# Kernel optimization log

Hardware: AMD Instinct MI355X
Metric: run time of the kernel (lower is better)

Reference implementation:

```python
import jax, jax.numpy as jnp
import numpy as np

N_NODES = 100000
N_EDGES = 1600000
D_IN = 128
D_OUT = 128


def setup_inputs() -> dict:
    key = jax.random.key(0)
    ks = jax.random.split(key, 8)
    x = jax.random.normal(ks[0], (N_NODES, D_IN), dtype=jnp.float32)
    edge_index = jax.random.randint(ks[1], (2, N_EDGES), 0, N_NODES, dtype=jnp.int64)
    s1 = 1.0 / np.sqrt(D_IN)
    s2 = 1.0 / np.sqrt(D_OUT)
    # SAGEConv: lin_l acts on aggregated neighbors (has bias), lin_r on self (no bias)
    Wl1 = jax.random.uniform(ks[2], (D_OUT, D_IN), jnp.float32, -s1, s1)
    Wr1 = jax.random.uniform(ks[3], (D_OUT, D_IN), jnp.float32, -s1, s1)
    b1 = jnp.zeros((D_OUT,), jnp.float32)
    Wl2 = jax.random.uniform(ks[4], (D_OUT, D_OUT), jnp.float32, -s2, s2)
    Wr2 = jax.random.uniform(ks[5], (D_OUT, D_OUT), jnp.float32, -s2, s2)
    b2 = jnp.zeros((D_OUT,), jnp.float32)
    return {"x": x, "edge_index": edge_index, "Wl1": Wl1, "Wr1": Wr1, "b1": b1,
            "Wl2": Wl2, "Wr2": Wr2, "b2": b2}


def _sage_conv(x, src, dst, Wl, Wr, b, n_nodes):
    # mean aggregation of source features at destination nodes
    agg = jax.ops.segment_sum(x[src], dst, num_segments=n_nodes)  # [N, d]
    deg = jax.ops.segment_sum(jnp.ones((src.shape[0],), x.dtype), dst, num_segments=n_nodes)
    mean = agg / jnp.maximum(deg, 1.0)[:, None]  # isolated nodes -> 0 (PyG scatter-mean)
    return mean @ Wl.T + b + x @ Wr.T


def reference(x, edge_index, Wl1, Wr1, b1, Wl2, Wr2, b2):
    src, dst = edge_index[0], edge_index[1]
    n = x.shape[0]
    h = _sage_conv(x, src, dst, Wl1, Wr1, b1, n)
    h = _sage_conv(h, src, dst, Wl2, Wr2, b2, n)
    return h
```

## Files before the change

kernel.cpp:

```cpp
#include <hip/hip_runtime.h>
#include <hip/hip_bf16.h>

#define D 128
#define SCAN_CHUNK 1024
#define TE 4096

typedef __attribute__((ext_vector_type(8))) short bf16x8;
typedef __attribute__((ext_vector_type(4))) float f32x4;
typedef __attribute__((ext_vector_type(2))) float f32x2;

__device__ __forceinline__ bool ei_is64(const int* ei32) {
    return (ei32[1] | ei32[3] | ei32[5] | ei32[7]) == 0;
}
__device__ __forceinline__ int get_idx(const void* ei, bool is64, long long pos) {
    return is64 ? (int)((const long long*)ei)[pos] : ((const int*)ei)[pos];
}

__global__ __launch_bounds__(256) void prep_kernel(
    const float* __restrict__ x, __hip_bfloat16* __restrict__ xb,
    unsigned* __restrict__ xq, long long ND, int ncvt,
    const float* __restrict__ Wl1, const float* __restrict__ Wr1,
    const float* __restrict__ Wl2, const float* __restrict__ Wr2,
    ushort* __restrict__ Wf1, ushort* __restrict__ Wf2,
    const void* __restrict__ ei, int E, int NB, int NBLK, int SH,
    int* __restrict__ histT) {
    __shared__ int h[512];
    const int t = threadIdx.x;
    int bid = blockIdx.x;

    if (bid < ncvt) {
        long long i = ((long long)bid * 256 + t) * 4;
        if (i + 3 < ND) {
            float4 v = *reinterpret_cast<const float4*>(x + i);
            __hip_bfloat16 o[4];
            o[0] = __float2bfloat16(v.x); o[1] = __float2bfloat16(v.y);
            o[2] = __float2bfloat16(v.z); o[3] = __float2bfloat16(v.w);
            *reinterpret_cast<ushort4*>(xb + i) = *reinterpret_cast<ushort4*>(o);
            int pk = __builtin_amdgcn_cvt_pk_fp8_f32(v.x, v.y, 0, false);
            pk = __builtin_amdgcn_cvt_pk_fp8_f32(v.z, v.w, pk, true);
            xq[i >> 2] = (unsigned)pk;
        } else {
            for (; i < ND; ++i) {
                float v = x[i];
                xb[i] = __float2bfloat16(v);
                int pk = __builtin_amdgcn_cvt_pk_fp8_f32(v, v, 0, false);
                ((unsigned char*)xq)[i] = (unsigned char)(pk & 0xff);
            }
        }
        return;
    }
    bid -= ncvt;
    if (bid < 32) {
        int gid = bid * 256 + t;
        int id = gid & 4095;
        const float* Wl = Wl1; const float* Wr = Wr1; ushort* Wf = Wf1;
        if (gid >= 4096) { Wl = Wl2; Wr = Wr2; Wf = Wf2; }
        int lane = id & 63, s = (id >> 6) & 7, j = id >> 9;
        int c = j * 16 + (lane & 15);
        int k = s * 32 + ((lane >> 4) << 3);
        const float* src = (k < 128) ? (Wl + c * 128 + k) : (Wr + c * 128 + (k - 128));
        float4 v0 = *reinterpret_cast<const float4*>(src);
        float4 v1 = *reinterpret_cast<const float4*>(src + 4);
        __hip_bfloat16 o[8];
        o[0] = __float2bfloat16(v0.x); o[1] = __float2bfloat16(v0.y);
        o[2] = __float2bfloat16(v0.z); o[3] = __float2bfloat16(v0.w);
        o[4] = __float2bfloat16(v1.x); o[5] = __float2bfloat16(v1.y);
        o[6] = __float2bfloat16(v1.z); o[7] = __float2bfloat16(v1.w);
        *reinterpret_cast<uint4*>(Wf + (size_t)id * 8) = *reinterpret_cast<uint4*>(o);
        return;
    }
    bid -= 32;
    for (int b = t; b < 512; b += 256) h[b] = 0;
    bool is64 = ei_is64((const int*)ei);
    __syncthreads();
    const int base = bid * TE;
    for (int i = t; i < TE; i += 256) {
        int e = base + i;
        if (e < E) {
            int d = get_idx(ei, is64, (long long)E + e);
            atomicAdd(&h[d >> SH], 1);
        }
    }
    __syncthreads();
    for (int b = t; b < NB; b += 256) histT[b * NBLK + bid] = h[b];
}

__global__ __launch_bounds__(256) void scan_partial_kernel(int* __restrict__ arr, int Ntot,
                                                           int* __restrict__ bsum) {
    __shared__ int s[SCAN_CHUNK];
    int base = blockIdx.x * SCAN_CHUNK;
    for (int j = threadIdx.x; j < SCAN_CHUNK; j += 256) {
        int i = base + j;
        s[j] = (i < Ntot) ? arr[i] : 0;
    }
    __syncthreads();
    if (threadIdx.x == 0) {
        int run = 0;
        for (int j = 0; j < SCAN_CHUNK; ++j) { int t = s[j]; s[j] = run; run += t; }
        bsum[blockIdx.x] = run;
    }
    __syncthreads();
    for (int j = threadIdx.x; j < SCAN_CHUNK; j += 256) {
        int i = base + j;
        if (i < Ntot) arr[i] = s[j];
    }
}

__global__ __launch_bounds__(256) void scan_top_kernel(int* __restrict__ bsum, int nb) {
    __shared__ int s[1024];
    const int t = threadIdx.x;
    for (int j = t; j < nb; j += 256) s[j] = bsum[j];
    __syncthreads();
    if (t == 0) {
        int run = 0;
        for (int j = 0; j < nb; ++j) { int v = s[j]; s[j] = run; run += v; }
    }
    __syncthreads();
    for (int j = t; j < nb; j += 256) bsum[j] = s[j];
}

__global__ __launch_bounds__(256) void part_scatter_kernel(const void* __restrict__ ei, int E,
                                                           int NB, int NBLK, int SH,
                                                           const int* __restrict__ histT,
                                                           const int* __restrict__ bsum,
                                                           unsigned* __restrict__ ebuf) {
    __shared__ int cur[512];
    const int t = threadIdx.x;
    bool is64 = ei_is64((const int*)ei);
    for (int b = t; b < NB; b += 256) {
        int idx = b * NBLK + blockIdx.x;
        cur[b] = histT[idx] + bsum[idx >> 10];
    }
    __syncthreads();
    const int base = blockIdx.x * TE;
    for (int i = t; i < TE; i += 256) {
        int e = base + i;
        if (e < E) {
            int s = get_idx(ei, is64, e);
            int d = get_idx(ei, is64, (long long)E + e);
            int pos = atomicAdd(&cur[d >> SH], 1);
            ebuf[pos] = (unsigned)s | ((unsigned)(d & ((1 << SH) - 1)) << 24);
        }
    }
}

__global__ __launch_bounds__(256) void bucket_csr_kernel(const unsigned* __restrict__ ebuf,
                                                         const int* __restrict__ histT,
                                                         const int* __restrict__ bsum,
                                                         int NB, int NBLK, int SH, int E,
                                                         int N, int* __restrict__ rs,
                                                         int* __restrict__ col) {
    const int b = blockIdx.x, t = threadIdx.x;
    const int nodes = 1 << SH;
    __shared__ int h[256];
    __shared__ int cur[256];
    __shared__ int sse[2];
    if (t == 0) {
        int i0 = b * NBLK;
        sse[0] = histT[i0] + bsum[i0 >> 10];
        if (b + 1 < NB) {
            int i1 = (b + 1) * NBLK;
            sse[1] = histT[i1] + bsum[i1 >> 10];
        } else {
            sse[1] = E;
        }
    }
    for (int l = t; l < nodes; l += 256) h[l] = 0;
    __syncthreads();
    const int bstart = sse[0], bend = sse[1];
    for (int i = bstart + t; i < bend; i += 256) {
        atomicAdd(&h[ebuf[i] >> 24], 1);
    }
    __syncthreads();
    for (int off = 1; off < nodes; off <<= 1) {
        int v = 0;
        if (t < nodes && t >= off) v = h[t - off];
        __syncthreads();
        if (t < nodes && t >= off) h[t] += v;
        __syncthreads();
    }
    const int node0 = b << SH;
    if (t < nodes) {
        int node = node0 + t;
        if (node < N) rs[node] = bstart + h[t];
        cur[t] = bstart + (t ? h[t - 1] : 0);
    }
    __syncthreads();
    for (int i = bstart + t; i < bend; i += 256) {
        unsigned ed = ebuf[i];
        int pos = atomicAdd(&cur[ed >> 24], 1);
        col[pos] = (int)(ed & 0xFFFFFFu);
    }
}

__global__ __launch_bounds__(256) void aggregate_mean_fp8_kernel(
    const unsigned char* __restrict__ xq, const int* __restrict__ rs,
    const int* __restrict__ col, ushort* __restrict__ outm, int N) {
    int t = threadIdx.x;
    int v = blockIdx.x * 4 + (t >> 6);
    if (v >= N) return;
    int lane = t & 63, q = lane >> 4, lc = lane & 15;
    int start = v ? rs[v - 1] : 0, end = rs[v];
    f32x2 a0 = {0.f, 0.f}, a1 = {0.f, 0.f}, a2 = {0.f, 0.f}, a3 = {0.f, 0.f};
    int e = start + q;
    for (; e + 4 < end; e += 8) {
        int s0 = col[e], s1 = col[e + 4];
        uint2 d0 = *reinterpret_cast<const uint2*>(xq + (size_t)s0 * D + lc * 8);
        uint2 d1 = *reinterpret_cast<const uint2*>(xq + (size_t)s1 * D + lc * 8);
        a0 += __builtin_amdgcn_cvt_pk_f32_fp8((int)d0.x, false);
        a1 += __builtin_amdgcn_cvt_pk_f32_fp8((int)d0.x, true);
        a2 += __builtin_amdgcn_cvt_pk_f32_fp8((int)d0.y, false);
        a3 += __builtin_amdgcn_cvt_pk_f32_fp8((int)d0.y, true);
        a0 += __builtin_amdgcn_cvt_pk_f32_fp8((int)d1.x, false);
        a1 += __builtin_amdgcn_cvt_pk_f32_fp8((int)d1.x, true);
        a2 += __builtin_amdgcn_cvt_pk_f32_fp8((int)d1.y, false);
        a3 += __builtin_amdgcn_cvt_pk_f32_fp8((int)d1.y, true);
    }
    if (e < end) {
        int s0 = col[e];
        uint2 d0 = *reinterpret_cast<const uint2*>(xq + (size_t)s0 * D + lc * 8);
        a0 += __builtin_amdgcn_cvt_pk_f32_fp8((int)d0.x, false);
        a1 += __builtin_amdgcn_cvt_pk_f32_fp8((int)d0.x, true);
        a2 += __builtin_amdgcn_cvt_pk_f32_fp8((int)d0.y, false);
        a3 += __builtin_amdgcn_cvt_pk_f32_fp8((int)d0.y, true);
    }
    float a[8] = {a0.x, a0.y, a1.x, a1.y, a2.x, a2.y, a3.x, a3.y};
#pragma unroll
    for (int i = 0; i < 8; ++i) {
        a[i] += __shfl_xor(a[i], 16);
        a[i] += __shfl_xor(a[i], 32);
    }
    if (q == 0) {
        float inv = (end > start) ? 1.0f / (float)(end - start) : 0.f;
        __hip_bfloat16 o[8];
#pragma unroll
        for (int i = 0; i < 8; ++i) o[i] = __float2bfloat16(a[i] * inv);
        *reinterpret_cast<uint4*>(outm + (size_t)v * D + lc * 8) =
            *reinterpret_cast<uint4*>(o);
    }
}

template <typename OutT, bool DUAL>
__global__ __launch_bounds__(512) void sage_mfma_kernel(
    const ushort* __restrict__ Ab, const ushort* __restrict__ Sb,
    const ushort* __restrict__ Wf, const float* __restrict__ bias,
    OutT* __restrict__ out, unsigned char* __restrict__ fq, int N) {
    __shared__ uint4 ldsB[4096];
    const int t = threadIdx.x;
    {
        const uint4* g = reinterpret_cast<const uint4*>(Wf);
#pragma unroll
        for (int i = 0; i < 8; ++i) ldsB[t + i * 512] = g[t + i * 512];
    }
    __syncthreads();

    const int lane = t & 63, w = t >> 6;
    const int lm = lane & 15;
    const int ksub = (lane >> 4) * 8;
    const int mbase = blockIdx.x * 128 + w * 16;

    int r0 = mbase + lm;
    if (r0 >= N) r0 = N - 1;

    f32x4 acc[8];
#pragma unroll
    for (int j = 0; j < 8; ++j) {
        float bv = bias[j * 16 + lm];
        acc[j] = {bv, bv, bv, bv};
    }

    const ushort* A0 = Ab + (size_t)r0 * D + ksub;
    const ushort* S0 = Sb + (size_t)r0 * D + ksub;
    const ushort* lB = reinterpret_cast<const ushort*>(ldsB) + lane * 8;

#pragma unroll
    for (int s = 0; s < 8; ++s) {
        bf16x8 a = (s < 4) ? *reinterpret_cast<const bf16x8*>(A0 + s * 32)
                           : *reinterpret_cast<const bf16x8*>(S0 + (s - 4) * 32);
#pragma unroll
        for (int j = 0; j < 8; ++j) {
            bf16x8 b = *reinterpret_cast<const bf16x8*>(lB + (j * 8 + s) * 512);
            acc[j] = __builtin_amdgcn_mfma_f32_16x16x32_bf16(a, b, acc[j], 0, 0, 0);
        }
    }

    const int rr = (lane >> 4) * 4;
#pragma unroll
    for (int r = 0; r < 4; ++r) {
        int row = mbase + rr + r;
        if (row < N) {
#pragma unroll
            for (int j = 0; j < 8; ++j) {
                float val = acc[j][r];
                if constexpr (sizeof(OutT) == 2)
                    out[(size_t)row * D + j * 16 + lm] = __float2bfloat16(val);
                else
                    out[(size_t)row * D + j * 16 + lm] = val;
                if constexpr (DUAL) {
                    int pk = __builtin_amdgcn_cvt_pk_fp8_f32(val, val, 0, false);
                    fq[(size_t)row * D + j * 16 + lm] = (unsigned char)(pk & 0xff);
                }
            }
        }
    }
}

extern "C" void kernel_launch(void* const* d_in, const int* in_sizes, int n_in,
                              void* d_out, int out_size, void* d_ws, size_t ws_size,
                              hipStream_t stream) {
    const float* x   = (const float*)d_in[0];
    const void*  ei  = d_in[1];
    const float* Wl1 = (const float*)d_in[2];
    const float* Wr1 = (const float*)d_in[3];
    const float* b1  = (const float*)d_in[4];
    const float* Wl2 = (const float*)d_in[5];
    const float* Wr2 = (const float*)d_in[6];
    const float* b2  = (const float*)d_in[7];
    float* out = (float*)d_out;

    const int N = in_sizes[0] / D;
    const int E = in_sizes[1] / 2;
    const long long ND = (long long)N * D;

    int SH = 8;
    while (((N + (1 << SH) - 1) >> SH) > 512) ++SH;
    const int NB = (N + (1 << SH) - 1) >> SH;
    const int NBLK = (E + TE - 1) / TE;
    const int Ntot = NB * NBLK;
    const int nb2 = (Ntot + SCAN_CHUNK - 1) / SCAN_CHUNK;

    ushort* meanb = (ushort*)d_ws;
    ushort* h1b   = meanb + ND;
    ushort* Wf1   = h1b + ND;
    ushort* Wf2   = Wf1 + 32768;
    int*    rs    = (int*)(Wf2 + 32768);
    int*    col   = rs + N;
    int*      histT = (int*)meanb;
    int*      bsum  = histT + Ntot;
    unsigned* ebuf  = (unsigned*)h1b;
    ushort*        xb  = (ushort*)d_out;
    unsigned char* xq  = (unsigned char*)d_out + 2 * ND;
    unsigned char* h1q = (unsigned char*)d_out + 3 * ND;

    const int ncvt = (int)((ND / 4 + 255) / 256);

    prep_kernel<<<ncvt + 32 + NBLK, 256, 0, stream>>>(
        x, (__hip_bfloat16*)xb, (unsigned*)xq, ND, ncvt, Wl1, Wr1, Wl2, Wr2,
        Wf1, Wf2, ei, E, NB, NBLK, SH, histT);

    scan_partial_kernel<<<nb2, 256, 0, stream>>>(histT, Ntot, bsum);
    scan_top_kernel<<<1, 256, 0, stream>>>(bsum, nb2);
    part_scatter_kernel<<<NBLK, 256, 0, stream>>>(ei, E, NB, NBLK, SH, histT, bsum, ebuf);
    bucket_csr_kernel<<<NB, 256, 0, stream>>>(ebuf, histT, bsum, NB, NBLK, SH, E, N, rs, col);

    const int agg_grid = (N + 3) / 4;
    const int gemm_grid = (N + 127) / 128;

    aggregate_mean_fp8_kernel<<<agg_grid, 256, 0, stream>>>(xq, rs, col, meanb, N);
    sage_mfma_kernel<__hip_bfloat16, true><<<gemm_grid, 512, 0, stream>>>(
        meanb, xb, Wf1, b1, (__hip_bfloat16*)h1b, h1q, N);

    aggregate_mean_fp8_kernel<<<agg_grid, 256, 0, stream>>>(h1q, rs, col, meanb, N);
    sage_mfma_kernel<float, false><<<gemm_grid, 512, 0, stream>>>(
        meanb, h1b, Wf2, b2, out, nullptr, N);
}
```

Baseline: 200.2 us.

## Drop bf16 copy of x and remap aggregation to one node per 16 lanes

The prep kernel no longer writes a bf16 copy of x. It only produces the fp8 copy, now 8 elements per thread. The first GEMM reads the fp32 x directly and converts it to bf16 in registers, which removes a full write and reread of a bf16 copy of x. The aggregation kernel now gives each node 16 lanes that walk every edge with 4-way unrolled gathers, instead of 64 lanes split into 4 edge groups joined by shuffles. This drops the cross-lane reduction and raises nodes per block, but each lane walks a longer serial edge chain and the first GEMM reads twice as many bytes for the self features.

After: 180.2 us. -10.0%, faster.

```diff
diff --git a/kernel.cpp b/kernel.cpp
--- a/kernel.cpp
+++ b/kernel.cpp
@@ -17,8 +17,7 @@
 }
 
 __global__ __launch_bounds__(256) void prep_kernel(
-    const float* __restrict__ x, __hip_bfloat16* __restrict__ xb,
-    unsigned* __restrict__ xq, long long ND, int ncvt,
+    const float* __restrict__ x, unsigned* __restrict__ xq, long long ND, int ncvt,
     const float* __restrict__ Wl1, const float* __restrict__ Wr1,
     const float* __restrict__ Wl2, const float* __restrict__ Wr2,
     ushort* __restrict__ Wf1, ushort* __restrict__ Wf2,
@@ -29,22 +28,20 @@
     int bid = blockIdx.x;
 
     if (bid < ncvt) {
-        long long i = ((long long)bid * 256 + t) * 4;
-        if (i + 3 < ND) {
-            float4 v = *reinterpret_cast<const float4*>(x + i);
-            __hip_bfloat16 o[4];
-            o[0] = __float2bfloat16(v.x); o[1] = __float2bfloat16(v.y);
-            o[2] = __float2bfloat16(v.z); o[3] = __float2bfloat16(v.w);
-            *reinterpret_cast<ushort4*>(xb + i) = *reinterpret_cast<ushort4*>(o);
-            int pk = __builtin_amdgcn_cvt_pk_fp8_f32(v.x, v.y, 0, false);
-            pk = __builtin_amdgcn_cvt_pk_fp8_f32(v.z, v.w, pk, true);
-            xq[i >> 2] = (unsigned)pk;
+        long long i = ((long long)bid * 256 + t) * 8;
+        if (i + 7 < ND) {
+            float4 v0 = *reinterpret_cast<const float4*>(x + i);
+            float4 v1 = *reinterpret_cast<const float4*>(x + i + 4);
+            int p0 = __builtin_amdgcn_cvt_pk_fp8_f32(v0.x, v0.y, 0, false);
+            p0 = __builtin_amdgcn_cvt_pk_fp8_f32(v0.z, v0.w, p0, true);
+            int p1 = __builtin_amdgcn_cvt_pk_fp8_f32(v1.x, v1.y, 0, false);
+            p1 = __builtin_amdgcn_cvt_pk_fp8_f32(v1.z, v1.w, p1, true);
+            *reinterpret_cast<uint2*>(reinterpret_cast<unsigned char*>(xq) + i) =
+                make_uint2((unsigned)p0, (unsigned)p1);
         } else {
             for (; i < ND; ++i) {
-                float v = x[i];
-                xb[i] = __float2bfloat16(v);
-                int pk = __builtin_amdgcn_cvt_pk_fp8_f32(v, v, 0, false);
-                ((unsigned char*)xq)[i] = (unsigned char)(pk & 0xff);
+                int pk = __builtin_amdgcn_cvt_pk_fp8_f32(x[i], x[i], 0, false);
+                reinterpret_cast<unsigned char*>(xq)[i] = (unsigned char)(pk & 0xff);
             }
         }
         return;
@@ -196,17 +193,20 @@
 __global__ __launch_bounds__(256) void aggregate_mean_fp8_kernel(
     const unsigned char* __restrict__ xq, const int* __restrict__ rs,
     const int* __restrict__ col, ushort* __restrict__ outm, int N) {
-    int t = threadIdx.x;
-    int v = blockIdx.x * 4 + (t >> 6);
+    const int t = threadIdx.x;
+    const int v = blockIdx.x * 16 + (t >> 4);
     if (v >= N) return;
-    int lane = t & 63, q = lane >> 4, lc = lane & 15;
-    int start = v ? rs[v - 1] : 0, end = rs[v];
+    const int lc = t & 15;
+    const int start = v ? rs[v - 1] : 0, end = rs[v];
+    const unsigned char* xbase = xq + lc * 8;
     f32x2 a0 = {0.f, 0.f}, a1 = {0.f, 0.f}, a2 = {0.f, 0.f}, a3 = {0.f, 0.f};
-    int e = start + q;
-    for (; e + 4 < end; e += 8) {
-        int s0 = col[e], s1 = col[e + 4];
-        uint2 d0 = *reinterpret_cast<const uint2*>(xq + (size_t)s0 * D + lc * 8);
-        uint2 d1 = *reinterpret_cast<const uint2*>(xq + (size_t)s1 * D + lc * 8);
+    int e = start;
+    for (; e + 3 < end; e += 4) {
+        int s0 = col[e], s1 = col[e + 1], s2 = col[e + 2], s3 = col[e + 3];
+        uint2 d0 = *reinterpret_cast<const uint2*>(xbase + (size_t)s0 * D);
+        uint2 d1 = *reinterpret_cast<const uint2*>(xbase + (size_t)s1 * D);
+        uint2 d2 = *reinterpret_cast<const uint2*>(xbase + (size_t)s2 * D);
+        uint2 d3 = *reinterpret_cast<const uint2*>(xbase + (size_t)s3 * D);
         a0 += __builtin_amdgcn_cvt_pk_f32_fp8((int)d0.x, false);
         a1 += __builtin_amdgcn_cvt_pk_f32_fp8((int)d0.x, true);
         a2 += __builtin_amdgcn_cvt_pk_f32_fp8((int)d0.y, false);
@@ -215,34 +215,36 @@
         a1 += __builtin_amdgcn_cvt_pk_f32_fp8((int)d1.x, true);
         a2 += __builtin_amdgcn_cvt_pk_f32_fp8((int)d1.y, false);
         a3 += __builtin_amdgcn_cvt_pk_f32_fp8((int)d1.y, true);
-    }
-    if (e < end) {
+        a0 += __builtin_amdgcn_cvt_pk_f32_fp8((int)d2.x, false);
+        a1 += __builtin_amdgcn_cvt_pk_f32_fp8((int)d2.x, true);
+        a2 += __builtin_amdgcn_cvt_pk_f32_fp8((int)d2.y, false);
+        a3 += __builtin_amdgcn_cvt_pk_f32_fp8((int)d2.y, true);
+        a0 += __builtin_amdgcn_cvt_pk_f32_fp8((int)d3.x, false);
+        a1 += __builtin_amdgcn_cvt_pk_f32_fp8((int)d3.x, true);
+        a2 += __builtin_amdgcn_cvt_pk_f32_fp8((int)d3.y, false);
+        a3 += __builtin_amdgcn_cvt_pk_f32_fp8((int)d3.y, true);
+    }
+    for (; e < end; ++e) {
         int s0 = col[e];
-        uint2 d0 = *reinterpret_cast<const uint2*>(xq + (size_t)s0 * D + lc * 8);
+        uint2 d0 = *reinterpret_cast<const uint2*>(xbase + (size_t)s0 * D);
         a0 += __builtin_amdgcn_cvt_pk_f32_fp8((int)d0.x, false);
         a1 += __builtin_amdgcn_cvt_pk_f32_fp8((int)d0.x, true);
         a2 += __builtin_amdgcn_cvt_pk_f32_fp8((int)d0.y, false);
         a3 += __builtin_amdgcn_cvt_pk_f32_fp8((int)d0.y, true);
     }
-    float a[8] = {a0.x, a0.y, a1.x, a1.y, a2.x, a2.y, a3.x, a3.y};
-#pragma unroll
-    for (int i = 0; i < 8; ++i) {
-        a[i] += __shfl_xor(a[i], 16);
-        a[i] += __shfl_xor(a[i], 32);
-    }
-    if (q == 0) {
-        float inv = (end > start) ? 1.0f / (float)(end - start) : 0.f;
-        __hip_bfloat16 o[8];
-#pragma unroll
-        for (int i = 0; i < 8; ++i) o[i] = __float2bfloat16(a[i] * inv);
-        *reinterpret_cast<uint4*>(outm + (size_t)v * D + lc * 8) =
-            *reinterpret_cast<uint4*>(o);
-    }
-}
-
-template <typename OutT, bool DUAL>
+    float inv = (end > start) ? 1.0f / (float)(end - start) : 0.f;
+    __hip_bfloat16 o[8];
+    o[0] = __float2bfloat16(a0.x * inv); o[1] = __float2bfloat16(a0.y * inv);
+    o[2] = __float2bfloat16(a1.x * inv); o[3] = __float2bfloat16(a1.y * inv);
+    o[4] = __float2bfloat16(a2.x * inv); o[5] = __float2bfloat16(a2.y * inv);
+    o[6] = __float2bfloat16(a3.x * inv); o[7] = __float2bfloat16(a3.y * inv);
+    *reinterpret_cast<uint4*>(outm + (size_t)v * D + lc * 8) =
+        *reinterpret_cast<uint4*>(o);
+}
+
+template <typename OutT, bool DUAL, bool SELFF32>
 __global__ __launch_bounds__(512) void sage_mfma_kernel(
-    const ushort* __restrict__ Ab, const ushort* __restrict__ Sb,
+    const ushort* __restrict__ Ab, const void* __restrict__ Sb,
     const ushort* __restrict__ Wf, const float* __restrict__ bias,
     OutT* __restrict__ out, unsigned char* __restrict__ fq, int N) {
     __shared__ uint4 ldsB[4096];
@@ -270,13 +272,27 @@
     }
 
     const ushort* A0 = Ab + (size_t)r0 * D + ksub;
-    const ushort* S0 = Sb + (size_t)r0 * D + ksub;
     const ushort* lB = reinterpret_cast<const ushort*>(ldsB) + lane * 8;
 
 #pragma unroll
     for (int s = 0; s < 8; ++s) {
-        bf16x8 a = (s < 4) ? *reinterpret_cast<const bf16x8*>(A0 + s * 32)
-                           : *reinterpret_cast<const bf16x8*>(S0 + (s - 4) * 32);
+        bf16x8 a;
+        if (s < 4) {
+            a = *reinterpret_cast<const bf16x8*>(A0 + s * 32);
+        } else if constexpr (SELFF32) {
+            const float* S0 = (const float*)Sb + (size_t)r0 * D + (s - 4) * 32 + ksub;
+            float4 v0 = *reinterpret_cast<const float4*>(S0);
+            float4 v1 = *reinterpret_cast<const float4*>(S0 + 4);
+            __hip_bfloat16 o[8];
+            o[0] = __float2bfloat16(v0.x); o[1] = __float2bfloat16(v0.y);
+            o[2] = __float2bfloat16(v0.z); o[3] = __float2bfloat16(v0.w);
+            o[4] = __float2bfloat16(v1.x); o[5] = __float2bfloat16(v1.y);
+            o[6] = __float2bfloat16(v1.z); o[7] = __float2bfloat16(v1.w);
+            a = *reinterpret_cast<bf16x8*>(o);
+        } else {
+            const ushort* S0 = (const ushort*)Sb + (size_t)r0 * D + ksub;
+            a = *reinterpret_cast<const bf16x8*>(S0 + (s - 4) * 32);
+        }
 #pragma unroll
         for (int j = 0; j < 8; ++j) {
             bf16x8 b = *reinterpret_cast<const bf16x8*>(lB + (j * 8 + s) * 512);
@@ -338,14 +354,13 @@
     int*      histT = (int*)meanb;
     int*      bsum  = histT + Ntot;
     unsigned* ebuf  = (unsigned*)h1b;
-    ushort*        xb  = (ushort*)d_out;
-    unsigned char* xq  = (unsigned char*)d_out + 2 * ND;
-    unsigned char* h1q = (unsigned char*)d_out + 3 * ND;
-
-    const int ncvt = (int)((ND / 4 + 255) / 256);
+    unsigned char* xq  = (unsigned char*)d_out;
+    unsigned char* h1q = (unsigned char*)d_out + ND;
+
+    const int ncvt = (int)((ND / 8 + 255) / 256);
 
     prep_kernel<<<ncvt + 32 + NBLK, 256, 0, stream>>>(
-        x, (__hip_bfloat16*)xb, (unsigned*)xq, ND, ncvt, Wl1, Wr1, Wl2, Wr2,
+        x, (unsigned*)xq, ND, ncvt, Wl1, Wr1, Wl2, Wr2,
         Wf1, Wf2, ei, E, NB, NBLK, SH, histT);
 
     scan_partial_kernel<<<nb2, 256, 0, stream>>>(histT, Ntot, bsum);
@@ -353,14 +368,14 @@
     part_scatter_kernel<<<NBLK, 256, 0, stream>>>(ei, E, NB, NBLK, SH, histT, bsum, ebuf);
     bucket_csr_kernel<<<NB, 256, 0, stream>>>(ebuf, histT, bsum, NB, NBLK, SH, E, N, rs, col);
 
-    const int agg_grid = (N + 3) / 4;
+    const int agg_grid = (N + 15) / 16;
     const int gemm_grid = (N + 127) / 128;
 
     aggregate_mean_fp8_kernel<<<agg_grid, 256, 0, stream>>>(xq, rs, col, meanb, N);
-    sage_mfma_kernel<__hip_bfloat16, true><<<gemm_grid, 512, 0, stream>>>(
-        meanb, xb, Wf1, b1, (__hip_bfloat16*)h1b, h1q, N);
+    sage_mfma_kernel<__hip_bfloat16, true, true><<<gemm_grid, 512, 0, stream>>>(
+        meanb, x, Wf1, b1, (__hip_bfloat16*)h1b, h1q, N);
 
     aggregate_mean_fp8_kernel<<<agg_grid, 256, 0, stream>>>(h1q, rs, col, meanb, N);
-    sage_mfma_kernel<float, false><<<gemm_grid, 512, 0, stream>>>(
+    sage_mfma_kernel<float, false, false><<<gemm_grid, 512, 0, stream>>>(
         meanb, h1b, Wf2, b2, out, nullptr, N);
 }
```
